# Kernel optimization log

Hardware: AMD Instinct MI355X
Metric: run time of the kernel (lower is better)

The kernel has to match this reference:

```python
import jax, jax.numpy as jnp
import numpy as np

D_MODEL = 1024
H = 16
D_K = D_MODEL // H  # 64
RANK = 5
ALPHA = 1.0


def _lora_linear(x, W, b, dW, dB):
    # merged weight: W + alpha * dB @ dW  (shape [out, in]); F.linear -> x @ W_merged.T + b
    Wm = W + ALPHA * (dB @ dW)
    return x @ Wm.T + b


def setup_inputs() -> dict:
    key = jax.random.key(0)
    ks = jax.random.split(key, 16)
    b_s, nq = 2, 2048
    s = 1.0 / np.sqrt(D_MODEL).astype(np.float32)
    inp = {
        "x": jax.random.normal(ks[0], (b_s, nq, D_MODEL), dtype=jnp.float32),
    }
    names = ["q", "k", "v", "o"]
    i = 1
    for n in names:
        inp[f"{n}_w"] = jax.random.normal(ks[i], (D_MODEL, D_MODEL), dtype=jnp.float32) * s; i += 1
        inp[f"{n}_b"] = jnp.zeros((D_MODEL,), dtype=jnp.float32)
        inp[f"{n}_dw"] = jax.random.normal(ks[i], (RANK, D_MODEL), dtype=jnp.float32) * 0.01; i += 1
        inp[f"{n}_db"] = jax.random.normal(ks[i], (D_MODEL, RANK), dtype=jnp.float32) * 0.01; i += 1
    return inp


def reference(x, q_w, q_b, q_dw, q_db, k_w, k_b, k_dw, k_db,
              v_w, v_b, v_dw, v_db, o_w, o_b, o_dw, o_db):
    b_s, nq, _ = x.shape
    q = _lora_linear(x, q_w, q_b, q_dw, q_db).reshape(b_s, nq, H, D_K)
    k = _lora_linear(x, k_w, k_b, k_dw, k_db).reshape(b_s, nq, H, D_K)
    v = _lora_linear(x, v_w, v_b, v_dw, v_db).reshape(b_s, nq, H, D_K)
    # scores: [b, h, q, k]
    att = jnp.einsum("bqhd,bkhd->bhqk", q, k) / np.sqrt(D_K).astype(np.float32)
    att = jax.nn.softmax(att, axis=-1)
    out = jnp.einsum("bhqk,bkhd->bqhd", att, v).reshape(b_s, nq, H * D_K)
    out = _lora_linear(out, o_w, o_b, o_dw, o_db)
    return out
```

## Files before the change

### kernel.cpp

```cpp
#include <hip/hip_runtime.h>
#include <hip/hip_bf16.h>

#define NQ 2048
#define NB 2

typedef unsigned short u16;
typedef unsigned int u32;
typedef _Float16 f16;
typedef __attribute__((ext_vector_type(8))) _Float16 half8;
typedef __attribute__((ext_vector_type(2))) __fp16 fp16x2;
typedef __attribute__((ext_vector_type(4))) float f32x4;
typedef __attribute__((ext_vector_type(2))) unsigned int u32x2;

#define MFMAH(A, B, C) __builtin_amdgcn_mfma_f32_16x16x32_f16(A, B, C, 0, 0, 0)

__device__ __forceinline__ u16 f2h(float x) {
    f16 h = (f16)x;
    return *(u16*)&h;
}
__device__ __forceinline__ u32 pk_h2(float a, float b) {
    union { fp16x2 v; u32 u; } c;
    c.v = __builtin_amdgcn_cvt_pkrtz(a, b);
    return c.u;
}
__device__ __forceinline__ float fexp2(float x) {
#if __has_builtin(__builtin_amdgcn_exp2f)
    return __builtin_amdgcn_exp2f(x);
#else
    return exp2f(x);
#endif
}
__device__ __forceinline__ void glds16(const u16* g, u16* l) {
    typedef const __attribute__((address_space(1))) u16 gu16;
    typedef __attribute__((address_space(3))) u16 lu16;
    __builtin_amdgcn_global_load_lds((gu16*)g, (lu16*)l, 16, 0, 0);
}
__device__ __forceinline__ void pl32swap(u32& a, u32& b) {
#if __has_builtin(__builtin_amdgcn_permlane32_swap)
    u32x2 r = __builtin_amdgcn_permlane32_swap(a, b, false, false);
    a = r[0]; b = r[1];
#else
    asm volatile("v_permlane32_swap_b32 %0, %1" : "+v"(a), "+v"(b));
#endif
}
__device__ __forceinline__ void pl16swap(u32& a, u32& b) {
#if __has_builtin(__builtin_amdgcn_permlane16_swap)
    u32x2 r = __builtin_amdgcn_permlane16_swap(a, b, false, false);
    a = r[0]; b = r[1];
#else
    asm volatile("v_permlane16_swap_b32 %0, %1" : "+v"(a), "+v"(b));
#endif
}

#define QSCALE 0.18033688011112042f

__global__ __launch_bounds__(256) void merge_w16(
    const float* __restrict__ w0, const float* __restrict__ dw0, const float* __restrict__ db0,
    const float* __restrict__ w1, const float* __restrict__ dw1, const float* __restrict__ db1,
    const float* __restrict__ w2, const float* __restrict__ dw2, const float* __restrict__ db2,
    const float* __restrict__ w3, const float* __restrict__ dw3, const float* __restrict__ db3,
    u16* __restrict__ Wf) {
    int i4 = (blockIdx.x * 256 + threadIdx.x) * 4;
    int row = i4 >> 10, col = i4 & 1023;
    int which = row >> 10, lr = row & 1023;
    const float* W  = (which == 0) ? w0  : (which == 1) ? w1  : (which == 2) ? w2  : w3;
    const float* dW = (which == 0) ? dw0 : (which == 1) ? dw1 : (which == 2) ? dw2 : dw3;
    const float* dB = (which == 0) ? db0 : (which == 1) ? db1 : (which == 2) ? db2 : db3;
    float4 acc = *(const float4*)&W[lr * 1024 + col];
#pragma unroll
    for (int r = 0; r < 5; ++r) {
        float s = dB[lr * 5 + r];
        float4 w4 = *(const float4*)&dW[r * 1024 + col];
        acc.x += s * w4.x; acc.y += s * w4.y;
        acc.z += s * w4.z; acc.w += s * w4.w;
    }
    if (which == 0) { acc.x *= QSCALE; acc.y *= QSCALE; acc.z *= QSCALE; acc.w *= QSCALE; }
    ushort4 o = make_ushort4(f2h(acc.x), f2h(acc.y), f2h(acc.z), f2h(acc.w));
    *(ushort4*)&Wf[i4] = o;
}

__global__ __launch_bounds__(256) void bias_pack(
    const float* __restrict__ b0, const float* __restrict__ b1,
    const float* __restrict__ b2, const float* __restrict__ b3,
    float* __restrict__ ball) {
    int t = blockIdx.x * 256 + threadIdx.x;
    int which = t >> 10;
    const float* B = (which == 0) ? b0 : (which == 1) ? b1 : (which == 2) ? b2 : b3;
    float v = B[t & 1023];
    if (which == 0) v *= QSCALE;
    ball[t] = v;
}

__global__ __launch_bounds__(256) void xcast(const float* __restrict__ x,
                                             u16* __restrict__ xf) {
    int i4 = (blockIdx.x * 256 + threadIdx.x) * 4;
    float4 v = *(const float4*)&x[i4];
    *(uint2*)&xf[i4] = make_uint2(pk_h2(v.x, v.y), pk_h2(v.z, v.w));
}

template <int TM>
__global__ __launch_bounds__(256) void gemm_f16(
    const u16* __restrict__ Af, const u16* __restrict__ Bf,
    const float* __restrict__ bias,
    float* __restrict__ Cf, u16* __restrict__ Cb, int ldc,
    u16* __restrict__ VtOut) {
    constexpr int MI = TM / 32;
    __shared__ u16 As[2][TM * 32];
    __shared__ u16 Bs[2][128 * 32];
    const int tid = threadIdx.x;
    const int wid = tid >> 6, lane = tid & 63;
    const int ln = lane & 15, quad = lane >> 4;
    const int bm = blockIdx.y * TM, bn = blockIdx.x * 128;
    const int wm = (wid >> 1) * (TM / 2), wn = (wid & 1) * 64;
    const int lrow = lane >> 2;
    const int lchunk = (lane & 3) * 8;

    f32x4 acc[MI][4];
#pragma unroll
    for (int i = 0; i < MI; ++i)
#pragma unroll
        for (int j = 0; j < 4; ++j) acc[i][j] = (f32x4){0.f, 0.f, 0.f, 0.f};

    for (int k0 = 0; k0 < 1024; k0 += 64) {
#pragma unroll
        for (int hf = 0; hf < 2; ++hf) {
#pragma unroll
            for (int p = 0; p < TM / 64; ++p) {
                int r = p * 64 + wid * 16;
                glds16(&Af[(bm + r + lrow) * 1024 + k0 + hf * 32 + lchunk],
                       &As[hf][r * 32]);
            }
#pragma unroll
            for (int p = 0; p < 2; ++p) {
                int r = p * 64 + wid * 16;
                glds16(&Bf[(bn + r + lrow) * 1024 + k0 + hf * 32 + lchunk],
                       &Bs[hf][r * 32]);
            }
        }
        asm volatile("s_waitcnt vmcnt(0)" ::: "memory");
        __syncthreads();

        half8 a[MI][2], b[4][2];
#pragma unroll
        for (int kc = 0; kc < 2; ++kc) {
#pragma unroll
            for (int j = 0; j < 4; ++j)
                b[j][kc] = *(const half8*)&Bs[kc][(wn + j * 16 + ln) * 32 + quad * 8];
#pragma unroll
            for (int i = 0; i < MI; ++i)
                a[i][kc] = *(const half8*)&As[kc][(wm + i * 16 + ln) * 32 + quad * 8];
        }
#pragma unroll
        for (int i = 0; i < MI; ++i)
#pragma unroll
            for (int j = 0; j < 4; ++j) {
                acc[i][j] = MFMAH(a[i][0], b[j][0], acc[i][j]);
                acc[i][j] = MFMAH(a[i][1], b[j][1], acc[i][j]);
            }
        __syncthreads();
    }

    if (VtOut && bn >= 2048) {
#pragma unroll
        for (int i = 0; i < MI; ++i)
#pragma unroll
            for (int j = 0; j < 4; ++j) {
                int col = bn + wn + j * 16 + ln;
                float bv = bias[col];
                int colV = col - 2048;
                int row0 = bm + wm + i * 16 + quad * 4;
                ushort4 pk = make_ushort4(f2h(acc[i][j][0] + bv), f2h(acc[i][j][1] + bv),
                                          f2h(acc[i][j][2] + bv), f2h(acc[i][j][3] + bv));
                *(ushort4*)&VtOut[colV * 4096 + row0] = pk;
            }
        return;
    }

#pragma unroll
    for (int i = 0; i < MI; ++i)
#pragma unroll
        for (int j = 0; j < 4; ++j) {
            int col = bn + wn + j * 16 + ln;
            float bv = bias[col];
#pragma unroll
            for (int r = 0; r < 4; ++r) {
                int row = bm + wm + i * 16 + quad * 4 + r;
                float v = acc[i][j][r] + bv;
                if (Cb) Cb[row * ldc + col] = f2h(v);
                else    Cf[row * ldc + col] = v;
            }
        }
}

__global__ __launch_bounds__(256) void flash_f16(
    const u16* __restrict__ QKV, const u16* __restrict__ Vt,
    u16* __restrict__ AO) {
    __shared__ u16 Ks[2][2][64 * 32];
    __shared__ u16 Vs[2][2][64 * 32];

    const int tid = threadIdx.x;
    const int wid = tid >> 6, lane = tid & 63;
    const int ln = lane & 15, quad = lane >> 4;
    const int qt = blockIdx.x, h = blockIdx.y, b = blockIdx.z;
    const int rowbase = b * NQ;
    const int col0 = h * 64;
    const int q0 = rowbase + qt * 128 + wid * 32;
    const int lrow = lane >> 2;
    const int lchunk = (lane & 3) * 8;

    const half8 ones = {(f16)1, (f16)1, (f16)1, (f16)1,
                        (f16)1, (f16)1, (f16)1, (f16)1};

    half8 qf[2][2];
#pragma unroll
    for (int mi = 0; mi < 2; ++mi)
#pragma unroll
        for (int kc = 0; kc < 2; ++kc)
            qf[mi][kc] = *(const half8*)&QKV[(q0 + mi * 16 + ln) * 3072 + col0 +
                                             kc * 32 + quad * 8];

    f32x4 accO[4][2];
    f32x4 accS[2];
#pragma unroll
    for (int mi = 0; mi < 2; ++mi) {
        accS[mi] = (f32x4){0.f, 0.f, 0.f, 0.f};
#pragma unroll
        for (int a = 0; a < 4; ++a) accO[a][mi] = (f32x4){0.f, 0.f, 0.f, 0.f};
    }

    const int NT = NQ / 64;
    const u16* Kg = QKV + (rowbase + wid * 16 + lrow) * 3072 + 1024 + col0 + lchunk;
    const u16* Vg = Vt + (col0 + wid * 16 + lrow) * 4096 + rowbase + lchunk;

#define STAGE(kt2, bu)                                         \
    {                                                          \
        const u16* kg_ = Kg + (kt2) * (64 * 3072);             \
        const u16* vg_ = Vg + (kt2) * 64;                      \
        glds16(kg_,      &Ks[bu][0][wid * 512]);               \
        glds16(kg_ + 32, &Ks[bu][1][wid * 512]);               \
        glds16(vg_,      &Vs[bu][0][wid * 512]);               \
        glds16(vg_ + 32, &Vs[bu][1][wid * 512]);               \
    }

    STAGE(0, 0);
    asm volatile("s_waitcnt vmcnt(0)" ::: "memory");
    __syncthreads();

#pragma unroll 2
    for (int kt = 0; kt < NT; ++kt) {
        const int cur = kt & 1;
        if (kt + 1 < NT) STAGE(kt + 1, cur ^ 1);

        f32x4 s[4][2];
#pragma unroll
        for (int a = 0; a < 4; ++a) {
            half8 kf0 = *(const half8*)&Ks[cur][0][(a * 16 + ln) * 32 + quad * 8];
            half8 kf1 = *(const half8*)&Ks[cur][1][(a * 16 + ln) * 32 + quad * 8];
#pragma unroll
            for (int mi = 0; mi < 2; ++mi) {
                f32x4 t = (f32x4){0.f, 0.f, 0.f, 0.f};
                t = MFMAH(kf0, qf[mi][0], t);
                t = MFMAH(kf1, qf[mi][1], t);
                s[a][mi] = t;
            }
        }

        half8 pf[2][2];
#pragma unroll
        for (int mi = 0; mi < 2; ++mi)
#pragma unroll
            for (int kc = 0; kc < 2; ++kc) {
                u32 c0 = pk_h2(fexp2(s[2 * kc][mi][0]), fexp2(s[2 * kc][mi][1]));
                u32 c1 = pk_h2(fexp2(s[2 * kc][mi][2]), fexp2(s[2 * kc][mi][3]));
                u32 c2 = pk_h2(fexp2(s[2 * kc + 1][mi][0]), fexp2(s[2 * kc + 1][mi][1]));
                u32 c3 = pk_h2(fexp2(s[2 * kc + 1][mi][2]), fexp2(s[2 * kc + 1][mi][3]));
                pl32swap(c0, c2);
                pl32swap(c1, c3);
                pl16swap(c0, c2);
                pl16swap(c1, c3);
                union { u32 u[4]; half8 h; } pu;
                pu.u[0] = c0; pu.u[1] = c1; pu.u[2] = c2; pu.u[3] = c3;
                pf[mi][kc] = pu.h;
                accS[mi] = MFMAH(ones, pf[mi][kc], accS[mi]);
            }

#pragma unroll
        for (int a = 0; a < 4; ++a) {
            half8 vf0 = *(const half8*)&Vs[cur][0][(a * 16 + ln) * 32 + quad * 8];
            half8 vf1 = *(const half8*)&Vs[cur][1][(a * 16 + ln) * 32 + quad * 8];
#pragma unroll
            for (int mi = 0; mi < 2; ++mi) {
                accO[a][mi] = MFMAH(vf0, pf[mi][0], accO[a][mi]);
                accO[a][mi] = MFMAH(vf1, pf[mi][1], accO[a][mi]);
            }
        }

        asm volatile("s_waitcnt vmcnt(0)" ::: "memory");
        __syncthreads();
    }
#undef STAGE

#pragma unroll
    for (int mi = 0; mi < 2; ++mi) {
        float inv = 1.f / accS[mi][0];
        int q = q0 + mi * 16 + ln;
#pragma unroll
        for (int a = 0; a < 4; ++a) {
            ushort4 pk = make_ushort4(f2h(accO[a][mi][0] * inv),
                                      f2h(accO[a][mi][1] * inv),
                                      f2h(accO[a][mi][2] * inv),
                                      f2h(accO[a][mi][3] * inv));
            *(ushort4*)&AO[q * 1024 + col0 + a * 16 + quad * 4] = pk;
        }
    }
}

extern "C" void kernel_launch(void* const* d_in, const int* in_sizes, int n_in,
                              void* d_out, int out_size, void* d_ws, size_t ws_size,
                              hipStream_t stream) {
    const float* x = (const float*)d_in[0];
    const float* w[4]  = {(const float*)d_in[1],  (const float*)d_in[5],
                          (const float*)d_in[9],  (const float*)d_in[13]};
    const float* bv[4] = {(const float*)d_in[2],  (const float*)d_in[6],
                          (const float*)d_in[10], (const float*)d_in[14]};
    const float* dw[4] = {(const float*)d_in[3],  (const float*)d_in[7],
                          (const float*)d_in[11], (const float*)d_in[15]};
    const float* db[4] = {(const float*)d_in[4],  (const float*)d_in[8],
                          (const float*)d_in[12], (const float*)d_in[16]};

    u16* p = (u16*)d_ws;
    u16* Wf  = p; p += 4096 * 1024;
    u16* xf  = p; p += 4096 * 1024;
    u16* QKV = p; p += 4096 * 3072;
    u16* Vt  = p; p += 1024 * 4096;
    float* ball = (float*)p;
    u16* AO = xf;

    merge_w16<<<4096, 256, 0, stream>>>(w[0], dw[0], db[0], w[1], dw[1], db[1],
                                        w[2], dw[2], db[2], w[3], dw[3], db[3], Wf);
    bias_pack<<<16, 256, 0, stream>>>(bv[0], bv[1], bv[2], bv[3], ball);
    xcast<<<4096, 256, 0, stream>>>(x, xf);

    gemm_f16<128><<<dim3(24, 32), 256, 0, stream>>>(xf, Wf, ball,
                                                    nullptr, QKV, 3072, Vt);

    flash_f16<<<dim3(NQ / 128, 16, NB), 256, 0, stream>>>(QKV, Vt, AO);

    gemm_f16<64><<<dim3(8, 64), 256, 0, stream>>>(AO, Wf + 3072 * 1024,
                                                  ball + 3072, (float*)d_out, nullptr, 1024,
                                                  nullptr);
}
```

Baseline: 227.8 us.

## Load V fragments directly from global and swizzle K LDS layout

```diff
diff --git a/kernel.cpp b/kernel.cpp
--- a/kernel.cpp
+++ b/kernel.cpp
@@ -196,7 +196,6 @@
     const u16* __restrict__ QKV, const u16* __restrict__ Vt,
     u16* __restrict__ AO) {
     __shared__ u16 Ks[2][2][64 * 32];
-    __shared__ u16 Vs[2][2][64 * 32];
 
     const int tid = threadIdx.x;
     const int wid = tid >> 6, lane = tid & 63;
@@ -206,7 +205,8 @@
     const int col0 = h * 64;
     const int q0 = rowbase + qt * 128 + wid * 32;
     const int lrow = lane >> 2;
-    const int lchunk = (lane & 3) * 8;
+    const int kchunk = ((lane & 3) ^ ((lrow >> 1) & 3)) * 8;
+    const int kswz = (quad ^ ((ln >> 1) & 3)) * 8;
 
     const half8 ones = {(f16)1, (f16)1, (f16)1, (f16)1,
                         (f16)1, (f16)1, (f16)1, (f16)1};
@@ -229,33 +229,37 @@
     }
 
     const int NT = NQ / 64;
-    const u16* Kg = QKV + (rowbase + wid * 16 + lrow) * 3072 + 1024 + col0 + lchunk;
-    const u16* Vg = Vt + (col0 + wid * 16 + lrow) * 4096 + rowbase + lchunk;
-
-#define STAGE(kt2, bu)                                         \
+    const u16* Kg = QKV + (rowbase + wid * 16 + lrow) * 3072 + 1024 + col0 + kchunk;
+    const u16* Vg = Vt + (col0 + ln) * 4096 + rowbase + quad * 8;
+
+#define STAGEK(kt2, bu)                                        \
     {                                                          \
         const u16* kg_ = Kg + (kt2) * (64 * 3072);             \
-        const u16* vg_ = Vg + (kt2) * 64;                      \
         glds16(kg_,      &Ks[bu][0][wid * 512]);               \
         glds16(kg_ + 32, &Ks[bu][1][wid * 512]);               \
-        glds16(vg_,      &Vs[bu][0][wid * 512]);               \
-        glds16(vg_ + 32, &Vs[bu][1][wid * 512]);               \
-    }
-
-    STAGE(0, 0);
+    }
+
+    STAGEK(0, 0);
     asm volatile("s_waitcnt vmcnt(0)" ::: "memory");
     __syncthreads();
 
 #pragma unroll 2
     for (int kt = 0; kt < NT; ++kt) {
         const int cur = kt & 1;
-        if (kt + 1 < NT) STAGE(kt + 1, cur ^ 1);
+        if (kt + 1 < NT) STAGEK(kt + 1, cur ^ 1);
+
+        half8 vf[4][2];
+#pragma unroll
+        for (int a = 0; a < 4; ++a)
+#pragma unroll
+            for (int hf = 0; hf < 2; ++hf)
+                vf[a][hf] = *(const half8*)&Vg[a * 16 * 4096 + kt * 64 + hf * 32];
 
         f32x4 s[4][2];
 #pragma unroll
         for (int a = 0; a < 4; ++a) {
-            half8 kf0 = *(const half8*)&Ks[cur][0][(a * 16 + ln) * 32 + quad * 8];
-            half8 kf1 = *(const half8*)&Ks[cur][1][(a * 16 + ln) * 32 + quad * 8];
+            half8 kf0 = *(const half8*)&Ks[cur][0][(a * 16 + ln) * 32 + kswz];
+            half8 kf1 = *(const half8*)&Ks[cur][1][(a * 16 + ln) * 32 + kswz];
 #pragma unroll
             for (int mi = 0; mi < 2; ++mi) {
                 f32x4 t = (f32x4){0.f, 0.f, 0.f, 0.f};
@@ -286,19 +290,17 @@
 
 #pragma unroll
         for (int a = 0; a < 4; ++a) {
-            half8 vf0 = *(const half8*)&Vs[cur][0][(a * 16 + ln) * 32 + quad * 8];
-            half8 vf1 = *(const half8*)&Vs[cur][1][(a * 16 + ln) * 32 + quad * 8];
 #pragma unroll
             for (int mi = 0; mi < 2; ++mi) {
-                accO[a][mi] = MFMAH(vf0, pf[mi][0], accO[a][mi]);
-                accO[a][mi] = MFMAH(vf1, pf[mi][1], accO[a][mi]);
+                accO[a][mi] = MFMAH(vf[a][0], pf[mi][0], accO[a][mi]);
+                accO[a][mi] = MFMAH(vf[a][1], pf[mi][1], accO[a][mi]);
             }
         }
 
         asm volatile("s_waitcnt vmcnt(0)" ::: "memory");
         __syncthreads();
     }
-#undef STAGE
+#undef STAGEK
 
 #pragma unroll
     for (int mi = 0; mi < 2; ++mi) {
```

New measurement: 254.1 us. 11.6% more time.
